# Kernel tuning notes

Measured on AMD Instinct MI355X. Metric: run time of the kernel, lower is better.

Reference implementation:

```python
import jax, jax.numpy as jnp
import numpy as np

B, S_CTX, S_Q, D_CTX, D_Q = 16, 2048, 2048, 1024, 1024
MASK_P = 0.1  # fraction of masked context positions


def setup_inputs() -> dict:
    key = jax.random.key(0)
    k1, k2, k3, k4 = jax.random.split(key, 4)
    context = jax.random.normal(k1, (B, S_CTX, D_CTX), dtype=jnp.float32)
    query = jax.random.normal(k2, (S_Q, B, D_Q), dtype=jnp.float32)  # [q_steps, batch, query_size]
    W = jax.random.normal(k3, (D_CTX, D_Q), dtype=jnp.float32)       # learned bilinear weights
    context_mask = jax.random.uniform(k4, (B, S_CTX)) < MASK_P       # True = masked position
    return {"context": context, "query": query, "W": W, "context_mask": context_mask}


def reference(context, query, W, context_mask):
    # scores[b, q, s] = context[b, s, :] @ W @ query[q, b, :]   (temp = 1.0, so no scaling)
    cw = jnp.einsum('bsd,de->bse', context, W)            # [B, S_ctx, D_q]
    scores = jnp.einsum('bse,qbe->bqs', cw, query)        # [B, S_q, S_ctx]
    neg = jnp.asarray(-1e30, scores.dtype)                # finite stand-in for -inf (NaN-safe)
    scores = jnp.where(context_mask[:, None, :], neg, scores)
    attn = jax.nn.softmax(scores, axis=2)                 # [B, S_q, S_ctx]
    # rows where the whole context is masked get attention zeroed out
    all_masked = jnp.all(context_mask, axis=1)[:, None, None]
    attn = jnp.where(all_masked, jnp.asarray(0.0, attn.dtype), attn)
    composition = jnp.einsum('bqs,bsd->qbd', attn, context)  # [S_q, B, D_ctx]
    attn_out = attn.transpose(1, 0, 2)                       # [S_q, B, S_ctx]
    return attn_out, composition
```

## Files before the change

### kernel.cpp

```cpp
#include <hip/hip_runtime.h>
#include <cmath>

#define B_  16
#define SEQ 2048
#define DIM 1024
#define LDST 40

typedef short  short8 __attribute__((ext_vector_type(8)));
typedef short  sh4    __attribute__((ext_vector_type(4)));
typedef float  f32x4  __attribute__((ext_vector_type(4)));

__device__ __forceinline__ unsigned short f2bf(float x) {
  unsigned u = __builtin_bit_cast(unsigned, x);
  return (unsigned short)((u + 0x7fffu + ((u >> 16) & 1u)) >> 16);
}
__device__ __forceinline__ float bf2f(unsigned short h) {
  unsigned u = ((unsigned)h) << 16;
  return __builtin_bit_cast(float, u);
}

__device__ __forceinline__ void gl16(const void* g, void* l) {
  __builtin_amdgcn_global_load_lds(
      (const __attribute__((address_space(1))) void*)g,
      (__attribute__((address_space(3))) void*)l, 16, 0, 0);
}

__global__ __launch_bounds__(256) void cvt_ctx(const float* __restrict__ X,
                                               unsigned short* __restrict__ hi,
                                               unsigned short* __restrict__ lo) {
  const size_t N8 = (size_t)B_ * SEQ * DIM / 8;
  for (size_t i = (size_t)blockIdx.x * 256 + threadIdx.x; i < N8;
       i += (size_t)gridDim.x * 256) {
    const size_t base = i * 8;
    float4 a = *(const float4*)&X[base];
    float4 c = *(const float4*)&X[base + 4];
    const float xs[8] = {a.x, a.y, a.z, a.w, c.x, c.y, c.z, c.w};
    short8 h, l;
#pragma unroll
    for (int j = 0; j < 8; ++j) {
      unsigned short hh = f2bf(xs[j]);
      h[j] = (short)hh;
      l[j] = (short)f2bf(xs[j] - bf2f(hh));
    }
    *(short8*)&hi[base] = h;
    *(short8*)&lo[base] = l;
  }
}

__global__ __launch_bounds__(256) void t_chi(const unsigned short* __restrict__ H,
                                             unsigned short* __restrict__ T) {
  __shared__ unsigned short L[64][72];
  const int t = threadIdx.x;
  const int d0 = blockIdx.x * 64, s0 = blockIdx.y * 64, b = blockIdx.z;
  const int sl = t >> 2, dp = (t & 3) * 16;
  short8 v0 = *(const short8*)&H[((size_t)b * SEQ + s0 + sl) * DIM + d0 + dp];
  short8 v1 = *(const short8*)&H[((size_t)b * SEQ + s0 + sl) * DIM + d0 + dp + 8];
  *(short8*)&L[sl][dp] = v0;
  *(short8*)&L[sl][dp + 8] = v1;
  __syncthreads();
  const int dl = t >> 2, sp = (t & 3) * 16;
  short8 o0, o1;
#pragma unroll
  for (int k = 0; k < 8; ++k) {
    o0[k] = (short)L[sp + k][dl];
    o1[k] = (short)L[sp + 8 + k][dl];
  }
  *(short8*)&T[((size_t)b * DIM + d0 + dl) * SEQ + s0 + sp] = o0;
  *(short8*)&T[((size_t)b * DIM + d0 + dl) * SEQ + s0 + sp + 8] = o1;
}

__global__ __launch_bounds__(256) void g1_z(const float* __restrict__ Q,
                                            const float* __restrict__ W,
                                            unsigned short* __restrict__ zhi,
                                            unsigned short* __restrict__ zlo) {
  __shared__ unsigned short Ah[128 * LDST], Al[128 * LDST];
  __shared__ unsigned short Bh[128 * LDST], Bl[128 * LDST];
  const int tid = threadIdx.x;
  const int m0 = blockIdx.y * 128, n0 = blockIdx.x * 128;
  const int wave = tid >> 6, lane = tid & 63;
  const int wm = (wave >> 1) * 64, wn = (wave & 1) * 64;
  const int rl = tid & 127;

  const float* srow = (tid < 128) ? Q + (size_t)(m0 + rl) * DIM
                                  : W + (size_t)(n0 + rl) * DIM;
  unsigned short* th = (tid < 128) ? Ah : Bh;
  unsigned short* tl = (tid < 128) ? Al : Bl;

  f32x4 acc[4][4];
#pragma unroll
  for (int i = 0; i < 4; ++i)
#pragma unroll
    for (int j = 0; j < 4; ++j) acc[i][j] = (f32x4){0.f, 0.f, 0.f, 0.f};

  for (int kc = 0; kc < DIM; kc += 32) {
    float4 fv[8];
#pragma unroll
    for (int j = 0; j < 8; ++j) fv[j] = *(const float4*)&srow[kc + j * 4];
    __syncthreads();
    short8 hv[4], lv[4];
#pragma unroll
    for (int j = 0; j < 8; ++j) {
      const float x[4] = {fv[j].x, fv[j].y, fv[j].z, fv[j].w};
#pragma unroll
      for (int c = 0; c < 4; ++c) {
        unsigned short h = f2bf(x[c]);
        unsigned short l = f2bf(x[c] - bf2f(h));
        hv[j >> 1][(j & 1) * 4 + c] = (short)h;
        lv[j >> 1][(j & 1) * 4 + c] = (short)l;
      }
    }
#pragma unroll
    for (int j = 0; j < 4; ++j) {
      *(short8*)&th[rl * LDST + j * 8] = hv[j];
      *(short8*)&tl[rl * LDST + j * 8] = lv[j];
    }
    __syncthreads();

    short8 ah[4], al[4], bh[4], bl[4];
#pragma unroll
    for (int f = 0; f < 4; ++f) {
      const int ao = (wm + f * 16 + (lane & 15)) * LDST + (lane >> 4) * 8;
      const int bo = (wn + f * 16 + (lane & 15)) * LDST + (lane >> 4) * 8;
      ah[f] = *(const short8*)&Ah[ao];  al[f] = *(const short8*)&Al[ao];
      bh[f] = *(const short8*)&Bh[bo];  bl[f] = *(const short8*)&Bl[bo];
    }
#pragma unroll
    for (int i = 0; i < 4; ++i)
#pragma unroll
      for (int j = 0; j < 4; ++j) {
        acc[i][j] = __builtin_amdgcn_mfma_f32_16x16x32_bf16(ah[i], bh[j], acc[i][j], 0, 0, 0);
        acc[i][j] = __builtin_amdgcn_mfma_f32_16x16x32_bf16(al[i], bh[j], acc[i][j], 0, 0, 0);
        acc[i][j] = __builtin_amdgcn_mfma_f32_16x16x32_bf16(ah[i], bl[j], acc[i][j], 0, 0, 0);
      }
  }
#pragma unroll
  for (int i = 0; i < 4; ++i)
#pragma unroll
    for (int j = 0; j < 4; ++j)
#pragma unroll
      for (int r = 0; r < 4; ++r) {
        const int row = m0 + wm + i * 16 + (lane >> 4) * 4 + r;
        const int col = n0 + wn + j * 16 + (lane & 15);
        const float v = acc[i][j][r];
        const unsigned short h = f2bf(v);
        zhi[(size_t)row * DIM + col] = h;
        zlo[(size_t)row * DIM + col] = f2bf(v - bf2f(h));
      }
}

#define G2GRID (16 * 16 * B_)
__global__ __launch_bounds__(256) void g2_scores(const unsigned short* __restrict__ zhi,
                                                 const unsigned short* __restrict__ zlo,
                                                 const unsigned short* __restrict__ chi,
                                                 const unsigned short* __restrict__ clo,
                                                 float* __restrict__ Sc) {
  __shared__ unsigned short Sh[128 * 32], Sl[128 * 32];
  __shared__ unsigned short Qh[128 * 32], Ql[128 * 32];
  const int tid = threadIdx.x, lane = tid & 63, wave = tid >> 6;

  const int lin = blockIdx.x;
  const int swz = (lin & 7) * (G2GRID / 8) + (lin >> 3);
  const int s0 = (swz & 15) * 128;
  const int q0 = ((swz >> 4) & 15) * 128;
  const int b  = swz >> 8;

  const int wm = (wave >> 1) * 64;
  const int wn = (wave & 1) * 64;

  const int r_sub = lane >> 2;
  const int c_sub = (((lane & 3) ^ ((lane >> 3) & 3))) * 8;

  f32x4 acc[4][4];
#pragma unroll
  for (int i = 0; i < 4; ++i)
#pragma unroll
    for (int j = 0; j < 4; ++j) acc[i][j] = (f32x4){0.f, 0.f, 0.f, 0.f};

  for (int kc = 0; kc < DIM; kc += 32) {
    if (wave == 0) {
#pragma unroll
      for (int it = 0; it < 8; ++it)
        gl16(&chi[((size_t)b * SEQ + s0 + it * 16 + r_sub) * DIM + kc + c_sub], &Sh[it * 512]);
    } else if (wave == 1) {
#pragma unroll
      for (int it = 0; it < 8; ++it)
        gl16(&clo[((size_t)b * SEQ + s0 + it * 16 + r_sub) * DIM + kc + c_sub], &Sl[it * 512]);
    } else if (wave == 2) {
#pragma unroll
      for (int it = 0; it < 8; ++it)
        gl16(&zhi[((size_t)(q0 + it * 16 + r_sub) * B_ + b) * DIM + kc + c_sub], &Qh[it * 512]);
    } else {
#pragma unroll
      for (int it = 0; it < 8; ++it)
        gl16(&zlo[((size_t)(q0 + it * 16 + r_sub) * B_ + b) * DIM + kc + c_sub], &Ql[it * 512]);
    }
    __syncthreads();

    short8 sh_[4], sl_[4], qh_[4], ql_[4];
#pragma unroll
    for (int f = 0; f < 4; ++f) {
      const int ra = wm + f * 16 + (lane & 15);
      const int rb = wn + f * 16 + (lane & 15);
      const int so = ra * 32 + (((lane >> 4) ^ ((ra >> 1) & 3))) * 8;
      const int qo = rb * 32 + (((lane >> 4) ^ ((rb >> 1) & 3))) * 8;
      sh_[f] = *(const short8*)&Sh[so];  sl_[f] = *(const short8*)&Sl[so];
      qh_[f] = *(const short8*)&Qh[qo];  ql_[f] = *(const short8*)&Ql[qo];
    }
#pragma unroll
    for (int i = 0; i < 4; ++i)
#pragma unroll
      for (int j = 0; j < 4; ++j) {
        acc[i][j] = __builtin_amdgcn_mfma_f32_16x16x32_bf16(sh_[i], qh_[j], acc[i][j], 0, 0, 0);
        acc[i][j] = __builtin_amdgcn_mfma_f32_16x16x32_bf16(sl_[i], qh_[j], acc[i][j], 0, 0, 0);
        acc[i][j] = __builtin_amdgcn_mfma_f32_16x16x32_bf16(sh_[i], ql_[j], acc[i][j], 0, 0, 0);
      }
    __syncthreads();
  }

#pragma unroll
  for (int i = 0; i < 4; ++i)
#pragma unroll
    for (int j = 0; j < 4; ++j) {
      const int s = s0 + wm + i * 16 + (lane >> 4) * 4;
      const int q = q0 + wn + j * 16 + (lane & 15);
      f32x4 v = {acc[i][j][0], acc[i][j][1], acc[i][j][2], acc[i][j][3]};
      __builtin_nontemporal_store(v, (f32x4*)&Sc[((size_t)q * B_ + b) * SEQ + s]);
    }
}

__global__ __launch_bounds__(256) void kernel_softmax(float* __restrict__ attn,
                                                      const int* __restrict__ mask) {
  const int row = blockIdx.x;
  const int b = row & (B_ - 1);
  float* p = attn + (size_t)row * SEQ;
  const int* m = mask + (size_t)b * SEQ;
  const int t = threadIdx.x;

  float4 va = *(const float4*)&p[t * 8];
  float4 vb = *(const float4*)&p[t * 8 + 4];
  int4 ma = *(const int4*)&m[t * 8];
  int4 mb = *(const int4*)&m[t * 8 + 4];
  float v[8] = {ma.x ? -1e30f : va.x, ma.y ? -1e30f : va.y,
                ma.z ? -1e30f : va.z, ma.w ? -1e30f : va.w,
                mb.x ? -1e30f : vb.x, mb.y ? -1e30f : vb.y,
                mb.z ? -1e30f : vb.z, mb.w ? -1e30f : vb.w};
  float mx = -INFINITY;
#pragma unroll
  for (int i = 0; i < 8; ++i) mx = fmaxf(mx, v[i]);
#pragma unroll
  for (int off = 32; off > 0; off >>= 1) mx = fmaxf(mx, __shfl_xor(mx, off));
  __shared__ float redmax[4];
  __shared__ float redsum[4];
  if ((t & 63) == 0) redmax[t >> 6] = mx;
  __syncthreads();
  mx = fmaxf(fmaxf(redmax[0], redmax[1]), fmaxf(redmax[2], redmax[3]));

  float sum = 0.f;
#pragma unroll
  for (int i = 0; i < 8; ++i) {
    v[i] = __expf(v[i] - mx);
    sum += v[i];
  }
#pragma unroll
  for (int off = 32; off > 0; off >>= 1) sum += __shfl_xor(sum, off);
  if ((t & 63) == 0) redsum[t >> 6] = sum;
  __syncthreads();
  sum = (redsum[0] + redsum[1]) + (redsum[2] + redsum[3]);

  const bool allmasked = (mx < -1e29f);
  const float inv = allmasked ? 0.f : 1.f / sum;
  float4 oa = {v[0] * inv, v[1] * inv, v[2] * inv, v[3] * inv};
  float4 ob = {v[4] * inv, v[5] * inv, v[6] * inv, v[7] * inv};
  *(float4*)&p[t * 8] = oa;
  *(float4*)&p[t * 8 + 4] = ob;
}

__global__ __launch_bounds__(256) void g3_comp(const float* __restrict__ attn,
                                               const unsigned short* __restrict__ ctxT,
                                               float* __restrict__ Out) {
  __shared__ unsigned short Ad[128 * 64];
  __shared__ unsigned short Bq[128 * 64];
  const int tid = threadIdx.x, lane = tid & 63, wave = tid >> 6;
  const int b = blockIdx.z;
  const int d0 = blockIdx.x * 128, q0 = blockIdx.y * 128;
  const int wm = (wave >> 1) * 64;
  const int wn = (wave & 1) * 64;

  const int r8 = lane >> 3;
  const int c8 = lane & 7;
  const unsigned short* agp =
      ctxT + ((size_t)b * DIM + d0 + wave * 32 + r8) * SEQ + (size_t)((c8 ^ r8) * 8);

  const int qrow = tid >> 1;
  const int rk = qrow & 7;
  const float* arow = attn + ((size_t)(q0 + qrow) * B_ + b) * SEQ + (tid & 1) * 32;

  f32x4 acc[4][4];
#pragma unroll
  for (int i = 0; i < 4; ++i)
#pragma unroll
    for (int j = 0; j < 4; ++j) acc[i][j] = (f32x4){0.f, 0.f, 0.f, 0.f};

  for (int kc = 0; kc < SEQ; kc += 64) {
    float4 fv[8];
#pragma unroll
    for (int jj = 0; jj < 8; ++jj) fv[jj] = *(const float4*)&arow[kc + jj * 4];
#pragma unroll
    for (int g = 0; g < 4; ++g)
      gl16(agp + (size_t)g * 8 * SEQ + kc, &Ad[(wave * 32 + g * 8) * 64]);
#pragma unroll
    for (int jw = 0; jw < 4; ++jw) {
      short8 w;
#pragma unroll
      for (int e = 0; e < 8; ++e) {
        const float4 f4 = fv[jw * 2 + (e >> 2)];
        const float x = (e & 3) == 0 ? f4.x : (e & 3) == 1 ? f4.y : (e & 3) == 2 ? f4.z : f4.w;
        w[e] = (short)f2bf(x);
      }
      const int blk = (tid & 1) * 4 + jw;
      *(short8*)&Bq[qrow * 64 + ((blk ^ rk)) * 8] = w;
    }
    __syncthreads();

    short8 af[4][2], bf_[4][2];
#pragma unroll
    for (int f = 0; f < 4; ++f) {
      const int ra = wm + f * 16 + (lane & 15);
      const int rb = wn + f * 16 + (lane & 15);
#pragma unroll
      for (int h = 0; h < 2; ++h) {
        const int kbA = h * 4 + (lane >> 4);
        af[f][h]  = *(const short8*)&Ad[ra * 64 + ((kbA ^ (ra & 7))) * 8];
        bf_[f][h] = *(const short8*)&Bq[rb * 64 + ((kbA ^ (rb & 7))) * 8];
      }
    }
#pragma unroll
    for (int i = 0; i < 4; ++i)
#pragma unroll
      for (int j = 0; j < 4; ++j) {
        acc[i][j] = __builtin_amdgcn_mfma_f32_16x16x32_bf16(af[i][0], bf_[j][0], acc[i][j], 0, 0, 0);
        acc[i][j] = __builtin_amdgcn_mfma_f32_16x16x32_bf16(af[i][1], bf_[j][1], acc[i][j], 0, 0, 0);
      }
    __syncthreads();
  }

#pragma unroll
  for (int i = 0; i < 4; ++i)
#pragma unroll
    for (int j = 0; j < 4; ++j) {
      const int d = d0 + wm + i * 16 + (lane >> 4) * 4;
      const int q = q0 + wn + j * 16 + (lane & 15);
      f32x4 v = {acc[i][j][0], acc[i][j][1], acc[i][j][2], acc[i][j][3]};
      __builtin_nontemporal_store(v, (f32x4*)&Out[((size_t)q * B_ + b) * DIM + d]);
    }
}

extern "C" void kernel_launch(void* const* d_in, const int* in_sizes, int n_in,
                              void* d_out, int out_size, void* d_ws, size_t ws_size,
                              hipStream_t stream) {
  const float* context = (const float*)d_in[0];
  const float* query   = (const float*)d_in[1];
  const float* W       = (const float*)d_in[2];
  const int*   mask    = (const int*)d_in[3];

  float* attn = (float*)d_out;
  float* comp = attn + (size_t)SEQ * B_ * SEQ;

  unsigned short* chi = (unsigned short*)comp;
  unsigned short* clo = chi + (size_t)B_ * SEQ * DIM;

  unsigned short* zhi  = (unsigned short*)d_ws;
  unsigned short* zlo  = zhi + (size_t)SEQ * B_ * DIM;
  unsigned short* ctxT = (unsigned short*)d_ws;

  cvt_ctx<<<dim3(4096), 256, 0, stream>>>(context, chi, clo);
  g1_z<<<dim3(DIM / 128, (SEQ * B_) / 128), 256, 0, stream>>>(query, W, zhi, zlo);
  g2_scores<<<dim3(G2GRID), 256, 0, stream>>>(zhi, zlo, chi, clo, attn);
  t_chi<<<dim3(DIM / 64, SEQ / 64, B_), 256, 0, stream>>>(chi, ctxT);
  kernel_softmax<<<dim3(SEQ * B_), 256, 0, stream>>>(attn, mask);
  g3_comp<<<dim3(DIM / 128, SEQ / 128, B_), 256, 0, stream>>>(attn, ctxT, comp);
}
```

Measured before the change: 1.308 ms.

## Pre-split query/W to bf16 hi/lo and feed GEMMs via direct LDS loads

Query and W are converted once into bf16 hi/lo buffers in scratch space, and the Z GEMM loads them through global_load_lds with an XOR-swizzled layout, a swizzled block order, and an added trailing barrier. Softmax now also writes a bf16 copy of attention in [b][q][s] layout, so the composition GEMM can stream both operands with direct LDS loads instead of reading fp32 and converting in registers. This removes the per-tile conversion ALU work and fp32 reads, at the cost of extra conversion passes and extra writes of bf16 intermediates.

```diff
diff --git a/kernel.cpp b/kernel.cpp
--- a/kernel.cpp
+++ b/kernel.cpp
@@ -4,7 +4,6 @@
 #define B_  16
 #define SEQ 2048
 #define DIM 1024
-#define LDST 40
 
 typedef short  short8 __attribute__((ext_vector_type(8)));
 typedef short  sh4    __attribute__((ext_vector_type(4)));
@@ -25,10 +24,32 @@
       (__attribute__((address_space(3))) void*)l, 16, 0, 0);
 }
 
-__global__ __launch_bounds__(256) void cvt_ctx(const float* __restrict__ X,
-                                               unsigned short* __restrict__ hi,
-                                               unsigned short* __restrict__ lo) {
+__global__ __launch_bounds__(256) void cvt_split(const float* __restrict__ X,
+                                                 unsigned short* __restrict__ hi,
+                                                 unsigned short* __restrict__ lo) {
   const size_t N8 = (size_t)B_ * SEQ * DIM / 8;
+  for (size_t i = (size_t)blockIdx.x * 256 + threadIdx.x; i < N8;
+       i += (size_t)gridDim.x * 256) {
+    const size_t base = i * 8;
+    float4 a = *(const float4*)&X[base];
+    float4 c = *(const float4*)&X[base + 4];
+    const float xs[8] = {a.x, a.y, a.z, a.w, c.x, c.y, c.z, c.w};
+    short8 h, l;
+#pragma unroll
+    for (int j = 0; j < 8; ++j) {
+      unsigned short hh = f2bf(xs[j]);
+      h[j] = (short)hh;
+      l[j] = (short)f2bf(xs[j] - bf2f(hh));
+    }
+    *(short8*)&hi[base] = h;
+    *(short8*)&lo[base] = l;
+  }
+}
+
+__global__ __launch_bounds__(256) void cvt_w(const float* __restrict__ X,
+                                             unsigned short* __restrict__ hi,
+                                             unsigned short* __restrict__ lo) {
+  const size_t N8 = (size_t)DIM * DIM / 8;
   for (size_t i = (size_t)blockIdx.x * 256 + threadIdx.x; i < N8;
        i += (size_t)gridDim.x * 256) {
     const size_t base = i * 8;
@@ -69,22 +90,27 @@
   *(short8*)&T[((size_t)b * DIM + d0 + dl) * SEQ + s0 + sp + 8] = o1;
 }
 
-__global__ __launch_bounds__(256) void g1_z(const float* __restrict__ Q,
-                                            const float* __restrict__ W,
+#define G1GRID 2048
+__global__ __launch_bounds__(256) void g1_z(const unsigned short* __restrict__ qh,
+                                            const unsigned short* __restrict__ ql,
+                                            const unsigned short* __restrict__ wh,
+                                            const unsigned short* __restrict__ wl,
                                             unsigned short* __restrict__ zhi,
                                             unsigned short* __restrict__ zlo) {
-  __shared__ unsigned short Ah[128 * LDST], Al[128 * LDST];
-  __shared__ unsigned short Bh[128 * LDST], Bl[128 * LDST];
-  const int tid = threadIdx.x;
-  const int m0 = blockIdx.y * 128, n0 = blockIdx.x * 128;
-  const int wave = tid >> 6, lane = tid & 63;
-  const int wm = (wave >> 1) * 64, wn = (wave & 1) * 64;
-  const int rl = tid & 127;
-
-  const float* srow = (tid < 128) ? Q + (size_t)(m0 + rl) * DIM
-                                  : W + (size_t)(n0 + rl) * DIM;
-  unsigned short* th = (tid < 128) ? Ah : Bh;
-  unsigned short* tl = (tid < 128) ? Al : Bl;
+  __shared__ unsigned short Ah[128 * 32], Al[128 * 32];
+  __shared__ unsigned short Bh[128 * 32], Bl[128 * 32];
+  const int tid = threadIdx.x, lane = tid & 63, wave = tid >> 6;
+
+  const int lin = blockIdx.x;
+  const int swz = (lin & 7) * (G1GRID / 8) + (lin >> 3);
+  const int m0 = (swz >> 3) * 128;
+  const int n0 = (swz & 7) * 128;
+
+  const int wm = (wave >> 1) * 64;
+  const int wn = (wave & 1) * 64;
+
+  const int r_sub = lane >> 2;
+  const int c_sub = (((lane & 3) ^ ((lane >> 3) & 3))) * 8;
 
   f32x4 acc[4][4];
 #pragma unroll
@@ -93,34 +119,32 @@
     for (int j = 0; j < 4; ++j) acc[i][j] = (f32x4){0.f, 0.f, 0.f, 0.f};
 
   for (int kc = 0; kc < DIM; kc += 32) {
-    float4 fv[8];
-#pragma unroll
-    for (int j = 0; j < 8; ++j) fv[j] = *(const float4*)&srow[kc + j * 4];
-    __syncthreads();
-    short8 hv[4], lv[4];
-#pragma unroll
-    for (int j = 0; j < 8; ++j) {
-      const float x[4] = {fv[j].x, fv[j].y, fv[j].z, fv[j].w};
-#pragma unroll
-      for (int c = 0; c < 4; ++c) {
-        unsigned short h = f2bf(x[c]);
-        unsigned short l = f2bf(x[c] - bf2f(h));
-        hv[j >> 1][(j & 1) * 4 + c] = (short)h;
-        lv[j >> 1][(j & 1) * 4 + c] = (short)l;
-      }
-    }
-#pragma unroll
-    for (int j = 0; j < 4; ++j) {
-      *(short8*)&th[rl * LDST + j * 8] = hv[j];
-      *(short8*)&tl[rl * LDST + j * 8] = lv[j];
+    if (wave == 0) {
+#pragma unroll
+      for (int it = 0; it < 8; ++it)
+        gl16(&qh[(size_t)(m0 + it * 16 + r_sub) * DIM + kc + c_sub], &Ah[it * 512]);
+    } else if (wave == 1) {
+#pragma unroll
+      for (int it = 0; it < 8; ++it)
+        gl16(&ql[(size_t)(m0 + it * 16 + r_sub) * DIM + kc + c_sub], &Al[it * 512]);
+    } else if (wave == 2) {
+#pragma unroll
+      for (int it = 0; it < 8; ++it)
+        gl16(&wh[(size_t)(n0 + it * 16 + r_sub) * DIM + kc + c_sub], &Bh[it * 512]);
+    } else {
+#pragma unroll
+      for (int it = 0; it < 8; ++it)
+        gl16(&wl[(size_t)(n0 + it * 16 + r_sub) * DIM + kc + c_sub], &Bl[it * 512]);
     }
     __syncthreads();
 
     short8 ah[4], al[4], bh[4], bl[4];
 #pragma unroll
     for (int f = 0; f < 4; ++f) {
-      const int ao = (wm + f * 16 + (lane & 15)) * LDST + (lane >> 4) * 8;
-      const int bo = (wn + f * 16 + (lane & 15)) * LDST + (lane >> 4) * 8;
+      const int ra = wm + f * 16 + (lane & 15);
+      const int rb = wn + f * 16 + (lane & 15);
+      const int ao = ra * 32 + (((lane >> 4) ^ ((ra >> 1) & 3))) * 8;
+      const int bo = rb * 32 + (((lane >> 4) ^ ((rb >> 1) & 3))) * 8;
       ah[f] = *(const short8*)&Ah[ao];  al[f] = *(const short8*)&Al[ao];
       bh[f] = *(const short8*)&Bh[bo];  bl[f] = *(const short8*)&Bl[bo];
     }
@@ -132,7 +156,9 @@
         acc[i][j] = __builtin_amdgcn_mfma_f32_16x16x32_bf16(al[i], bh[j], acc[i][j], 0, 0, 0);
         acc[i][j] = __builtin_amdgcn_mfma_f32_16x16x32_bf16(ah[i], bl[j], acc[i][j], 0, 0, 0);
       }
-  }
+    __syncthreads();
+  }
+
 #pragma unroll
   for (int i = 0; i < 4; ++i)
 #pragma unroll
@@ -229,11 +255,14 @@
 }
 
 __global__ __launch_bounds__(256) void kernel_softmax(float* __restrict__ attn,
-                                                      const int* __restrict__ mask) {
+                                                      const int* __restrict__ mask,
+                                                      unsigned short* __restrict__ attnb) {
   const int row = blockIdx.x;
   const int b = row & (B_ - 1);
+  const int q = row >> 4;
   float* p = attn + (size_t)row * SEQ;
   const int* m = mask + (size_t)b * SEQ;
+  unsigned short* pb = attnb + ((size_t)b * SEQ + q) * SEQ;
   const int t = threadIdx.x;
 
   float4 va = *(const float4*)&p[t * 8];
@@ -269,13 +298,21 @@
 
   const bool allmasked = (mx < -1e29f);
   const float inv = allmasked ? 0.f : 1.f / sum;
-  float4 oa = {v[0] * inv, v[1] * inv, v[2] * inv, v[3] * inv};
-  float4 ob = {v[4] * inv, v[5] * inv, v[6] * inv, v[7] * inv};
+  float o[8];
+  short8 ob16;
+#pragma unroll
+  for (int i = 0; i < 8; ++i) {
+    o[i] = v[i] * inv;
+    ob16[i] = (short)f2bf(o[i]);
+  }
+  float4 oa = {o[0], o[1], o[2], o[3]};
+  float4 ob = {o[4], o[5], o[6], o[7]};
   *(float4*)&p[t * 8] = oa;
   *(float4*)&p[t * 8 + 4] = ob;
-}
-
-__global__ __launch_bounds__(256) void g3_comp(const float* __restrict__ attn,
+  *(short8*)&pb[t * 8] = ob16;
+}
+
+__global__ __launch_bounds__(256) void g3_comp(const unsigned short* __restrict__ attnb,
                                                const unsigned short* __restrict__ ctxT,
                                                float* __restrict__ Out) {
   __shared__ unsigned short Ad[128 * 64];
@@ -288,12 +325,12 @@
 
   const int r8 = lane >> 3;
   const int c8 = lane & 7;
-  const unsigned short* agp =
-      ctxT + ((size_t)b * DIM + d0 + wave * 32 + r8) * SEQ + (size_t)((c8 ^ r8) * 8);
-
-  const int qrow = tid >> 1;
-  const int rk = qrow & 7;
-  const float* arow = attn + ((size_t)(q0 + qrow) * B_ + b) * SEQ + (tid & 1) * 32;
+  const unsigned short* src;
+  if (wave < 2)
+    src = ctxT + ((size_t)b * DIM + d0 + wave * 64 + r8) * SEQ + (size_t)((c8 ^ r8) * 8);
+  else
+    src = attnb + ((size_t)b * SEQ + q0 + (wave - 2) * 64 + r8) * SEQ + (size_t)((c8 ^ r8) * 8);
+  unsigned short* ldst = (wave < 2) ? &Ad[wave * 64 * 64] : &Bq[(wave - 2) * 64 * 64];
 
   f32x4 acc[4][4];
 #pragma unroll
@@ -302,24 +339,9 @@
     for (int j = 0; j < 4; ++j) acc[i][j] = (f32x4){0.f, 0.f, 0.f, 0.f};
 
   for (int kc = 0; kc < SEQ; kc += 64) {
-    float4 fv[8];
-#pragma unroll
-    for (int jj = 0; jj < 8; ++jj) fv[jj] = *(const float4*)&arow[kc + jj * 4];
-#pragma unroll
-    for (int g = 0; g < 4; ++g)
-      gl16(agp + (size_t)g * 8 * SEQ + kc, &Ad[(wave * 32 + g * 8) * 64]);
-#pragma unroll
-    for (int jw = 0; jw < 4; ++jw) {
-      short8 w;
-#pragma unroll
-      for (int e = 0; e < 8; ++e) {
-        const float4 f4 = fv[jw * 2 + (e >> 2)];
-        const float x = (e & 3) == 0 ? f4.x : (e & 3) == 1 ? f4.y : (e & 3) == 2 ? f4.z : f4.w;
-        w[e] = (short)f2bf(x);
-      }
-      const int blk = (tid & 1) * 4 + jw;
-      *(short8*)&Bq[qrow * 64 + ((blk ^ rk)) * 8] = w;
-    }
+#pragma unroll
+    for (int g = 0; g < 8; ++g)
+      gl16(src + (size_t)g * 8 * SEQ + kc, ldst + g * 8 * 64);
     __syncthreads();
 
     short8 af[4][2], bf_[4][2];
@@ -329,9 +351,9 @@
       const int rb = wn + f * 16 + (lane & 15);
 #pragma unroll
       for (int h = 0; h < 2; ++h) {
-        const int kbA = h * 4 + (lane >> 4);
-        af[f][h]  = *(const short8*)&Ad[ra * 64 + ((kbA ^ (ra & 7))) * 8];
-        bf_[f][h] = *(const short8*)&Bq[rb * 64 + ((kbA ^ (rb & 7))) * 8];
+        const int kb = h * 4 + (lane >> 4);
+        af[f][h]  = *(const short8*)&Ad[ra * 64 + ((kb ^ (ra & 7))) * 8];
+        bf_[f][h] = *(const short8*)&Bq[rb * 64 + ((kb ^ (rb & 7))) * 8];
       }
     }
 #pragma unroll
@@ -369,14 +391,22 @@
   unsigned short* chi = (unsigned short*)comp;
   unsigned short* clo = chi + (size_t)B_ * SEQ * DIM;
 
-  unsigned short* zhi  = (unsigned short*)d_ws;
-  unsigned short* zlo  = zhi + (size_t)SEQ * B_ * DIM;
-  unsigned short* ctxT = (unsigned short*)d_ws;
-
-  cvt_ctx<<<dim3(4096), 256, 0, stream>>>(context, chi, clo);
-  g1_z<<<dim3(DIM / 128, (SEQ * B_) / 128), 256, 0, stream>>>(query, W, zhi, zlo);
+  unsigned short* qh = (unsigned short*)attn;
+  unsigned short* ql = qh + (size_t)SEQ * B_ * DIM;
+  unsigned short* wh = ql + (size_t)SEQ * B_ * DIM;
+  unsigned short* wl = wh + (size_t)DIM * DIM;
+
+  unsigned short* zhi   = (unsigned short*)d_ws;
+  unsigned short* zlo   = zhi + (size_t)SEQ * B_ * DIM;
+  unsigned short* ctxT  = (unsigned short*)d_ws;
+  unsigned short* attnb = zlo;
+
+  cvt_split<<<dim3(4096), 256, 0, stream>>>(context, chi, clo);
+  cvt_split<<<dim3(4096), 256, 0, stream>>>(query, qh, ql);
+  cvt_w<<<dim3(512), 256, 0, stream>>>(W, wh, wl);
+  g1_z<<<dim3(G1GRID), 256, 0, stream>>>(qh, ql, wh, wl, zhi, zlo);
   g2_scores<<<dim3(G2GRID), 256, 0, stream>>>(zhi, zlo, chi, clo, attn);
   t_chi<<<dim3(DIM / 64, SEQ / 64, B_), 256, 0, stream>>>(chi, ctxT);
-  kernel_softmax<<<dim3(SEQ * B_), 256, 0, stream>>>(attn, mask);
-  g3_comp<<<dim3(DIM / 128, SEQ / 128, B_), 256, 0, stream>>>(attn, ctxT, comp);
-}
+  kernel_softmax<<<dim3(SEQ * B_), 256, 0, stream>>>(attn, mask, attnb);
+  g3_comp<<<dim3(DIM / 128, SEQ / 128, B_), 256, 0, stream>>>(attnb, ctxT, comp);
+}
```

After: 1.093 ms (median of 2 runs). 16.4% less time.
